# Optimization experiments

Hardware: AMD Instinct MI355X
Metric: run time of the kernel (lower is better)

## Reference

```python
import jax, jax.numpy as jnp
import numpy as np

WS = 2          # spatial window (patch) size
C = 96          # patch channels
IMG = 256       # image size
NS = IMG // WS  # 128 patches per side
N = NS * NS     # 16384 tokens
TD = C * WS * WS  # 384 token dim
H = 6           # heads
D = TD // H     # 64 head dim
W1 = 128        # one-sided attention window (attention_window=256 // 2)
G = 50          # num global tokens
NEG = -1e9
GPOS = np.linspace(0, N - 1, G).astype(np.int32)  # torch.linspace(...).long()


def setup_inputs() -> dict:
    key = jax.random.key(0)
    ks = jax.random.split(key, 13)
    s = 1.0 / np.sqrt(TD)
    def W(k):
        return jax.random.normal(k, (TD, TD), jnp.float32) * s
    def b(k):
        return jax.random.normal(k, (TD,), jnp.float32) * 0.02
    return {
        'x': jax.random.normal(ks[0], (2, C, IMG, IMG), jnp.float32),
        'Wq': W(ks[1]), 'bq': b(ks[2]),
        'Wk': W(ks[3]), 'bk': b(ks[4]),
        'Wv': W(ks[5]), 'bv': b(ks[6]),
        'Wqg': W(ks[7]), 'bqg': b(ks[8]),
        'Wkg': W(ks[9]), 'bkg': b(ks[10]),
        'Wvg': W(ks[11]), 'bvg': b(ks[12]),
    }


def _tokens(x):
    # (B,C,IMG,IMG) -> (B,N,TD); matches unfold/permute/view of the torch code
    B = x.shape[0]
    t = x.reshape(B, C, NS, WS, NS, WS).transpose(0, 1, 2, 4, 3, 5)  # B,C,ns,ns,ws,ws
    t = t.reshape(B, C, N, WS * WS).transpose(0, 2, 1, 3)
    return t.reshape(B, N, TD)


def _untokens(o):
    B = o.shape[0]
    o = o.reshape(B, NS, NS, C, WS, WS).transpose(0, 3, 1, 4, 2, 5)
    return o.reshape(B, C, IMG, IMG)


def _heads(t):
    B = t.shape[0]
    return t.reshape(B, -1, H, D).transpose(0, 2, 1, 3)  # (B,H,S,D)


def _longformer(tokens, Wq, bq, Wk, bk, Wv, bv, Wqg, bqg, Wkg, bkg, Wvg, bvg):
    B = tokens.shape[0]
    scale = np.float32(1.0 / np.sqrt(D))
    q = _heads(tokens @ Wq + bq) * scale  # (B,H,N,D)
    k = _heads(tokens @ Wk + bk)
    v = _heads(tokens @ Wv + bv)

    nc = N // W1  # 128 chunks of size w
    qc = q.reshape(B, H, nc, W1, D)
    # overlapping key/value chunks of size 3w (prev | cur | next)
    kp = jnp.pad(k, ((0, 0), (0, 0), (W1, W1), (0, 0))).reshape(B, H, nc + 2, W1, D)
    vp = jnp.pad(v, ((0, 0), (0, 0), (W1, W1), (0, 0))).reshape(B, H, nc + 2, W1, D)
    k3 = jnp.concatenate([kp[:, :, :-2], kp[:, :, 1:-1], kp[:, :, 2:]], axis=3)  # (B,H,nc,3w,D)
    v3 = jnp.concatenate([vp[:, :, :-2], vp[:, :, 1:-1], vp[:, :, 2:]], axis=3)

    band = jnp.einsum('bhcqd,bhckd->bhcqk', qc, k3)  # (B,H,nc,w,3w)
    # banded validity: key within +-w of query, and inside [0,N)
    i = np.arange(W1)[:, None]
    j = np.arange(3 * W1)[None, :]
    rel = j - W1 - i
    relmask = (rel >= -W1) & (rel <= W1)  # (w,3w)
    absidx = np.arange(nc)[:, None] * W1 + np.arange(3 * W1)[None, :] - W1
    absmask = (absidx >= 0) & (absidx < N)  # (nc,3w)
    mask = jnp.asarray(relmask[None, :, :] & absmask[:, None, :])  # (nc,w,3w)
    band = jnp.where(mask[None, None], band, NEG)

    # global key columns seen by every (local) query
    kg = k[:, :, GPOS]  # (B,H,G,D)
    vg = v[:, :, GPOS]
    gsc = jnp.einsum('bhcqd,bhgd->bhcqg', qc, kg)  # (B,H,nc,w,G)

    probs = jax.nn.softmax(jnp.concatenate([gsc, band], axis=-1), axis=-1)
    out = jnp.einsum('bhcqg,bhgd->bhcqd', probs[..., :G], vg) \
        + jnp.einsum('bhcqk,bhckd->bhcqd', probs[..., G:], v3)
    out = out.reshape(B, H, N, D).transpose(0, 2, 1, 3).reshape(B, N, TD)

    # global-query full attention (separate projections), overwrite global rows
    qg = _heads((tokens[:, GPOS] @ Wqg + bqg)) * scale  # (B,H,G,D)
    kga = _heads(tokens @ Wkg + bkg)  # (B,H,N,D)
    vga = _heads(tokens @ Wvg + bvg)
    gp = jax.nn.softmax(jnp.einsum('bhgd,bhnd->bhgn', qg, kga), axis=-1)
    og = jnp.einsum('bhgn,bhnd->bhgd', gp, vga).transpose(0, 2, 1, 3).reshape(B, G, TD)
    return out.at[:, GPOS].set(og)


def reference(x, Wq, bq, Wk, bk, Wv, bv, Wqg, bqg, Wkg, bkg, Wvg, bvg):
    tokens = _tokens(x)
    out = _longformer(tokens, Wq, bq, Wk, bk, Wv, bv, Wqg, bqg, Wkg, bkg, Wvg, bvg)
    return _untokens(out)
```

## Files before the change

kernel.cpp:

```cpp
#include <hip/hip_runtime.h>

#define DEVI __device__ __forceinline__

typedef __bf16 v8bf __attribute__((ext_vector_type(8)));
typedef float f32x4 __attribute__((ext_vector_type(4)));
typedef int int4v __attribute__((ext_vector_type(4)));
typedef int int2v __attribute__((ext_vector_type(2)));

constexpr int B_  = 2;
constexpr int C_  = 96;
constexpr int IMG = 256;
constexpr int N_  = 16384;
constexpr int TD  = 384;
constexpr int H_  = 6;
constexpr int G_  = 50;

DEVI short f2bf(float f){
  unsigned u = __builtin_bit_cast(unsigned, f);
  u = (u + 0x7fffu + ((u >> 16) & 1u)) >> 16;
  return (short)u;
}
DEVI unsigned cvtpk(float lo, float hi){
  unsigned r;
  asm("v_cvt_pk_bf16_f32 %0, %1, %2" : "=v"(r) : "v"(lo), "v"(hi));
  return r;
}
DEVI int gpos(int g){ return (16383 * g) / 49; }

DEVI f32x4 mfma16(v8bf a, v8bf b, f32x4 c){
  return __builtin_amdgcn_mfma_f32_16x16x32_bf16(a, b, c, 0, 0, 0);
}

DEVI void gload16(const void* g, void* l){
  __builtin_amdgcn_global_load_lds((const __attribute__((address_space(1))) void*)g,
                                   (__attribute__((address_space(3))) void*)l, 16, 0, 0);
}

__global__ __launch_bounds__(256) void prep_w(
    const float* __restrict__ w0, const float* __restrict__ w1,
    const float* __restrict__ w2, const float* __restrict__ w3,
    const float* __restrict__ w4, const float* __restrict__ w5,
    short* __restrict__ Wt){
  __shared__ float sT[64][65];
  int z = blockIdx.y;
  const float* W = z==0 ? w0 : z==1 ? w1 : z==2 ? w2 : z==3 ? w3 : z==4 ? w4 : w5;
  int tile = blockIdx.x;
  int k0 = (tile / 6) * 64, n0 = (tile % 6) * 64;
  int t = threadIdx.x;
  int r = t >> 2, c0 = (t & 3) * 16;
  #pragma unroll
  for (int e = 0; e < 16; e += 4){
    f32x4 v = *reinterpret_cast<const f32x4*>(&W[(size_t)(k0+r)*TD + n0 + c0 + e]);
    #pragma unroll
    for (int i = 0; i < 4; i++) sT[r][c0 + e + i] = v[i];
  }
  __syncthreads();
  int rn = t >> 2, ck0 = (t & 3) * 16;
  short pk[16];
  #pragma unroll
  for (int e = 0; e < 16; e++) pk[e] = f2bf(sT[ck0 + e][rn]);
  short* dst = Wt + (size_t)z*TD*TD + (size_t)(n0+rn)*TD + k0 + ck0;
  *reinterpret_cast<int4v*>(dst)     = *reinterpret_cast<int4v*>(&pk[0]);
  *reinterpret_cast<int4v*>(dst + 8) = *reinterpret_cast<int4v*>(&pk[8]);
}

__global__ void tokenize(const float* __restrict__ x, short* __restrict__ tokens){
  int idx = blockIdx.x * 256 + threadIdx.x;
  int t8 = idx % (TD/8);
  int bn = idx / (TD/8);
  int n = bn % N_, b = bn / N_;
  int t0 = t8 * 8;
  int i0 = (n >> 7) * 2, j0 = (n & 127) * 2;
  short o[8];
  #pragma unroll
  for (int e = 0; e < 8; e++){
    int t = t0 + e;
    int c = t >> 2, wi = (t >> 1) & 1, wj = t & 1;
    o[e] = f2bf(x[((b*C_ + c)*IMG + i0 + wi)*IMG + j0 + wj]);
  }
  *reinterpret_cast<int4v*>(tokens + bn*TD + t0) = *reinterpret_cast<int4v*>(o);
}

__global__ void gather_tokg(const short* __restrict__ tokens, short* __restrict__ tokg){
  int idx = blockIdx.x*256 + threadIdx.x;
  int r = idx / 48, cb = (idx % 48)*8;
  int b = r >> 6, q = r & 63;
  int4v val = {};
  if (q < G_) val = *reinterpret_cast<const int4v*>(tokens + ((size_t)b*N_ + gpos(q))*TD + cb);
  *reinterpret_cast<int4v*>(tokg + r*TD + cb) = val;
}

__global__ __launch_bounds__(256) void gemm_proj(
    const short* __restrict__ A, const short* __restrict__ Wt,
    const float* __restrict__ bq, const float* __restrict__ bk, const float* __restrict__ bv,
    const float* __restrict__ bkg, const float* __restrict__ bvg,
    short* __restrict__ qbuf, short* __restrict__ kbuf, short* __restrict__ vT,
    short* __restrict__ kgabuf, short* __restrict__ vgaT)
{
  __shared__ short smem[16384];
  int lin = blockIdx.x;
  int id = (lin & 7)*480 + (lin >> 3);
  int mt = id / 15, r15 = id % 15;
  int by = r15 % 3, bz = r15 / 3;
  const float* bias = bz==0 ? bq : bz==1 ? bk : bz==2 ? bv : bz==3 ? bkg : bvg;
  const short* Wz = Wt + bz*TD*TD;
  int m0 = mt * 128, n0 = by * 128;
  int tid = threadIdx.x, l = tid & 63, w = tid >> 6;
  int wm = w >> 1, wn = w & 1;
  int q16 = l & 15, g4 = l >> 4;

  int st_r  = (l >> 2);
  int st_cg = ((l & 3) ^ ((l >> 3) & 3));
  auto STAGE = [&](int kt, int s){
    #pragma unroll
    for (int it = 0; it < 4; it++){
      int ch = w*4 + it;
      int c8 = ch & 7;
      int r_ = c8*16 + st_r;
      const short* src = (ch < 8)
        ? A  + (size_t)(m0+r_)*TD + kt*32 + st_cg*8
        : Wz + (size_t)(n0+r_)*TD + kt*32 + st_cg*8;
      gload16(src, smem + ((ch < 8) ? 0 : 8192) + s*4096 + c8*512);
    }
  };

  int fr = q16;
  int fcg = g4 ^ ((l >> 1) & 3);
  f32x4 acc[4][4] = {};
  bool trans = (bz == 2 || bz == 4);

  STAGE(0, 0);
  if (trans){
    #pragma unroll 2
    for (int t = 0; t < 12; t++){
      int cur = t & 1;
      if (t < 11){ STAGE(t+1, cur ^ 1); asm volatile("s_waitcnt vmcnt(4)" ::: "memory"); }
      else       { asm volatile("s_waitcnt vmcnt(0)" ::: "memory"); }
      __builtin_amdgcn_s_barrier();
      v8bf af[4], bfr[4];
      #pragma unroll
      for (int i = 0; i < 4; i++){
        af[i]  = *reinterpret_cast<const v8bf*>(&smem[       cur*4096 + (wm*64 + i*16 + fr)*32 + fcg*8]);
        bfr[i] = *reinterpret_cast<const v8bf*>(&smem[8192 + cur*4096 + (wn*64 + i*16 + fr)*32 + fcg*8]);
      }
      #pragma unroll
      for (int mi = 0; mi < 4; mi++)
        #pragma unroll
        for (int ni = 0; ni < 4; ni++)
          acc[mi][ni] = mfma16(af[mi], bfr[ni], acc[mi][ni]);
      asm volatile("s_waitcnt lgkmcnt(0)" ::: "memory");
      __builtin_amdgcn_s_barrier();
    }
    short* outT = (bz == 2) ? vT : vgaT;
    #pragma unroll
    for (int mi = 0; mi < 4; mi++){
      int n_base = wm*64 + mi*16 + g4*4;
      #pragma unroll
      for (int ni = 0; ni < 4; ni++){
        int t_local = wn*64 + ni*16 + q16;
        float bc = bias[n0 + t_local];
        short pk[4];
        #pragma unroll
        for (int jj = 0; jj < 4; jj++) pk[jj] = f2bf(acc[mi][ni][jj] + bc);
        int phys = t_local*128 + (((n_base >> 3) ^ (t_local & 15)) << 3) + (n_base & 7);
        *reinterpret_cast<int2v*>(&smem[phys]) = *reinterpret_cast<int2v*>(pk);
      }
    }
    __syncthreads();
    int b = mt >> 7;
    int nb = m0 & 16383;
    #pragma unroll
    for (int p = 0; p < 8; p++){
      int t = p*16 + (tid >> 4);
      int c8 = tid & 15;
      int4v val = *reinterpret_cast<const int4v*>(&smem[t*128 + ((c8 ^ (t & 15)) << 3)]);
      int h = (n0 + t) >> 6, d = (n0 + t) & 63;
      *reinterpret_cast<int4v*>(outT + ((size_t)((b*H_ + h)*64 + d))*N_ + nb + c8*8) = val;
    }
  } else {
    #pragma unroll 2
    for (int t = 0; t < 12; t++){
      int cur = t & 1;
      if (t < 11){ STAGE(t+1, cur ^ 1); asm volatile("s_waitcnt vmcnt(4)" ::: "memory"); }
      else       { asm volatile("s_waitcnt vmcnt(0)" ::: "memory"); }
      __builtin_amdgcn_s_barrier();
      v8bf af[4], bfr[4];
      #pragma unroll
      for (int i = 0; i < 4; i++){
        af[i]  = *reinterpret_cast<const v8bf*>(&smem[       cur*4096 + (wm*64 + i*16 + fr)*32 + fcg*8]);
        bfr[i] = *reinterpret_cast<const v8bf*>(&smem[8192 + cur*4096 + (wn*64 + i*16 + fr)*32 + fcg*8]);
      }
      #pragma unroll
      for (int mi = 0; mi < 4; mi++)
        #pragma unroll
        for (int ni = 0; ni < 4; ni++)
          acc[mi][ni] = mfma16(bfr[ni], af[mi], acc[mi][ni]);
      asm volatile("s_waitcnt lgkmcnt(0)" ::: "memory");
      __builtin_amdgcn_s_barrier();
    }
    short* out = bz==0 ? qbuf : bz==1 ? kbuf : kgabuf;
    float scale = (bz == 0) ? 0.125f : 1.0f;
    #pragma unroll
    for (int mi = 0; mi < 4; mi++){
      int tl = wm*64 + mi*16 + q16;
      int x = (tl & 7) << 1;
      #pragma unroll
      for (int ni = 0; ni < 4; ni++){
        int tdl = wn*64 + ni*16 + g4*4;
        f32x4 bvv = *reinterpret_cast<const f32x4*>(&bias[n0 + tdl]);
        short pk[4];
        #pragma unroll
        for (int jj = 0; jj < 4; jj++) pk[jj] = f2bf((acc[mi][ni][jj] + bvv[jj]) * scale);
        int c4 = (tdl >> 2) ^ x;
        *reinterpret_cast<int2v*>(&smem[tl*128 + c4*4]) = *reinterpret_cast<int2v*>(pk);
      }
    }
    __syncthreads();
    #pragma unroll
    for (int p = 0; p < 8; p++){
      int r = p*16 + (tid >> 4);
      int c16 = tid & 15;
      int c4 = (2*c16) ^ ((r & 7) << 1);
      int4v val = *reinterpret_cast<const int4v*>(&smem[r*128 + c4*4]);
      *reinterpret_cast<int4v*>(out + (size_t)(m0 + r)*TD + n0 + c16*8) = val;
    }
  }
}

__global__ __launch_bounds__(256) void gemm_qg(
    const short* __restrict__ A, const short* __restrict__ Wt,
    const float* __restrict__ bias, short* __restrict__ out)
{
  __shared__ short sA[128][72];
  __shared__ short sB[128][72];
  const short* Wz = Wt + 5*TD*TD;
  int n0 = blockIdx.x * 128;
  int tid = threadIdx.x, l = tid & 63, w = tid >> 6;
  int wm = w >> 1, wn = w & 1;
  f32x4 acc[4][4] = {};
  for (int k0 = 0; k0 < TD; k0 += 64){
    #pragma unroll
    for (int i = 0; i < 4; i++){
      int ch = i*256 + tid; int row = ch >> 3, cb = (ch & 7) * 8;
      *reinterpret_cast<int4v*>(&sA[row][cb]) = *reinterpret_cast<const int4v*>(A  + row*TD + k0 + cb);
      *reinterpret_cast<int4v*>(&sB[row][cb]) = *reinterpret_cast<const int4v*>(Wz + (n0+row)*TD + k0 + cb);
    }
    __syncthreads();
    #pragma unroll
    for (int ks = 0; ks < 2; ks++){
      v8bf af[4], bfr[4];
      #pragma unroll
      for (int i = 0; i < 4; i++){
        af[i]  = *reinterpret_cast<const v8bf*>(&sA[wm*64 + i*16 + (l&15)][ks*32 + (l>>4)*8]);
        bfr[i] = *reinterpret_cast<const v8bf*>(&sB[wn*64 + i*16 + (l&15)][ks*32 + (l>>4)*8]);
      }
      #pragma unroll
      for (int mi = 0; mi < 4; mi++)
        #pragma unroll
        for (int ni = 0; ni < 4; ni++)
          acc[mi][ni] = mfma16(af[mi], bfr[ni], acc[mi][ni]);
    }
    __syncthreads();
  }
  #pragma unroll
  for (int mi = 0; mi < 4; mi++){
    int row = wm*64 + mi*16 + (l>>4)*4;
    #pragma unroll
    for (int ni = 0; ni < 4; ni++){
      int col = n0 + wn*64 + ni*16 + (l&15);
      float bc = bias[col];
      #pragma unroll
      for (int jj = 0; jj < 4; jj++)
        out[(row+jj)*TD + col] = f2bf((acc[mi][ni][jj] + bc) * 0.125f);
    }
  }
}

__global__ void gather_gkv(const short* __restrict__ kbuf, const short* __restrict__ vT,
                           short* __restrict__ kg, short* __restrict__ vgTg){
  int bh = blockIdx.x; int b = bh / H_, h = bh % H_;
  int t = threadIdx.x;
  #pragma unroll
  for (int it = 0; it < 2; it++){
    int u = it*256 + t; int g = u >> 3, cc = (u & 7)*8;
    int4v val = {};
    if (g < G_) val = *reinterpret_cast<const int4v*>(kbuf + ((size_t)b*N_ + gpos(g))*TD + h*64 + cc);
    *reinterpret_cast<int4v*>(kg + (size_t)bh*4096 + g*64 + cc) = val;
  }
  #pragma unroll
  for (int it = 0; it < 16; it++){
    int u = it*256 + t; int d = u >> 6, g = u & 63;
    short val = 0;
    if (g < G_) val = vT[((size_t)bh*64 + d)*N_ + gpos(g)];
    vgTg[(size_t)bh*4096 + d*64 + g] = val;
  }
}

__global__ __launch_bounds__(512, 4) void band_attn(
    const short* __restrict__ qb, const short* __restrict__ kbuf, const short* __restrict__ vT,
    const short* __restrict__ kg, const short* __restrict__ vgTg,
    float* __restrict__ out)
{
  __shared__ short sK[448][64];
  __shared__ short sP[8][16][72];
  int lin = blockIdx.y*128 + blockIdx.x;
  int id = (lin & 7)*192 + (lin >> 3);
  int c = id & 127;
  int bh = id >> 7; int b = bh / H_, h = bh % H_;
  int tid = threadIdx.x, l = tid & 63, w = tid >> 6;
  int g4 = l >> 4, q16 = l & 15;
  int cb0 = c*128 - 128;

  #pragma unroll
  for (int it = 0; it < 7; it++){
    int ch = w*7 + it;
    int r = ch*8 + (l>>3);
    int cc = ((l & 7) ^ (l >> 3)) * 8;
    const short* src;
    if (ch < 8){
      src = kg + (size_t)bh*4096 + r*64 + cc;
    } else {
      int ka = cb0 + r - 64;
      ka = ka < 0 ? 0 : (ka > N_-1 ? N_-1 : ka);
      src = kbuf + ((size_t)b*N_ + ka)*TD + h*64 + cc;
    }
    gload16(src, &sK[ch*8][0]);
  }

  int qrow0 = c*128 + w*16;
  v8bf aq[2];
  #pragma unroll
  for (int s = 0; s < 2; s++)
    aq[s] = *reinterpret_cast<const v8bf*>(qb + ((size_t)b*N_ + qrow0 + q16)*TD + h*64 + s*32 + g4*8);

  __syncthreads();

  f32x4 o[4] = {};
  float mrun = -1e30f, lrun = 0.f;

  int sbase = w >> 2;
  for (int sidx = 0; sidx < 6; sidx++){
    bool isg = (sidx == 0);
    int s0b = (sbase + sidx - 1) * 64;
    int kabs0 = cb0 + s0b;
    if (!isg && (kabs0 < 0 || kabs0 >= N_)) continue;
    int rbase = isg ? 0 : 64 + s0b;
    v8bf bv0[4];
    #pragma unroll
    for (int cf = 0; cf < 4; cf++){
      const short* vsrc = isg
        ? vgTg + (size_t)bh*4096 + (cf*16 + q16)*64 + g4*8
        : vT + ((size_t)bh*64 + cf*16 + q16)*N_ + kabs0 + g4*8;
      bv0[cf] = *reinterpret_cast<const v8bf*>(vsrc);
    }
    v8bf bkf[4][2];
    #pragma unroll
    for (int kc = 0; kc < 4; kc++)
      #pragma unroll
      for (int s = 0; s < 2; s++)
        bkf[kc][s] = *reinterpret_cast<const v8bf*>(
            &sK[rbase + kc*16 + q16][(((s << 2) | g4) ^ (q16 & 7)) * 8]);
    f32x4 sc[4] = {};
    __builtin_amdgcn_s_setprio(1);
    #pragma unroll
    for (int kc = 0; kc < 4; kc++){
      sc[kc] = mfma16(bkf[kc][0], aq[0], sc[kc]);
      sc[kc] = mfma16(bkf[kc][1], aq[1], sc[kc]);
    }
    __builtin_amdgcn_s_setprio(0);
    if (isg){
      #pragma unroll
      for (int jj = 0; jj < 4; jj++)
        if (48 + g4*4 + jj >= G_) sc[3][jj] = -1e30f;
    } else {
      bool allv = (s0b >= w*16 + 15) && (s0b <= w*16 + 193);
      if (!allv){
        int i_ = w*16 + q16;
        #pragma unroll
        for (int kc = 0; kc < 4; kc++)
          #pragma unroll
          for (int jj = 0; jj < 4; jj++){
            int rel = s0b + kc*16 + g4*4 + jj - 128 - i_;
            if (rel < -128 || rel > 128) sc[kc][jj] = -1e30f;
          }
      }
    }
    float mk = -1e30f;
    #pragma unroll
    for (int kc = 0; kc < 4; kc++)
      #pragma unroll
      for (int jj = 0; jj < 4; jj++) mk = fmaxf(mk, sc[kc][jj]);
    mk = fmaxf(mk, __shfl_xor(mk, 16, 64));
    mk = fmaxf(mk, __shfl_xor(mk, 32, 64));
    float mnew = fmaxf(mrun, mk);
    float f_ = __expf(mrun - mnew);
    mrun = mnew;
    float s_ = 0.f;
    #pragma unroll
    for (int kc = 0; kc < 4; kc++){
      #pragma unroll
      for (int jj = 0; jj < 4; jj++){
        sc[kc][jj] = __expf(sc[kc][jj] - mnew);
        s_ += sc[kc][jj];
      }
      int2v pw = { (int)cvtpk(sc[kc][0], sc[kc][1]), (int)cvtpk(sc[kc][2], sc[kc][3]) };
      *reinterpret_cast<int2v*>(&sP[w][q16][kc*16 + g4*4]) = pw;
    }
    s_ += __shfl_xor(s_, 16, 64);
    s_ += __shfl_xor(s_, 32, 64);
    lrun = lrun*f_ + s_;
    #pragma unroll
    for (int cf = 0; cf < 4; cf++)
      #pragma unroll
      for (int jj = 0; jj < 4; jj++) o[cf][jj] *= f_;
    v8bf ap[2];
    #pragma unroll
    for (int s2 = 0; s2 < 2; s2++)
      ap[s2] = *reinterpret_cast<const v8bf*>(&sP[w][q16][s2*32 + g4*8]);
    v8bf bv1[4];
    #pragma unroll
    for (int cf = 0; cf < 4; cf++){
      const short* vsrc = isg
        ? vgTg + (size_t)bh*4096 + (cf*16 + q16)*64 + 32 + g4*8
        : vT + ((size_t)bh*64 + cf*16 + q16)*N_ + kabs0 + 32 + g4*8;
      bv1[cf] = *reinterpret_cast<const v8bf*>(vsrc);
    }
    __builtin_amdgcn_s_setprio(1);
    #pragma unroll
    for (int cf = 0; cf < 4; cf++) o[cf] = mfma16(bv0[cf], ap[0], o[cf]);
    #pragma unroll
    for (int cf = 0; cf < 4; cf++) o[cf] = mfma16(bv1[cf], ap[1], o[cf]);
    __builtin_amdgcn_s_setprio(0);
  }
  float inv = 1.0f / lrun;
  int n = qrow0 + q16;
  int i0 = (n >> 7)*2, j0 = (n & 127)*2;
  #pragma unroll
  for (int cf = 0; cf < 4; cf++)
    #pragma unroll
    for (int jj = 0; jj < 4; jj++){
      float val = o[cf][jj] * inv;
      int t_ = h*64 + cf*16 + g4*4 + jj;
      int cc = t_ >> 2, wi = (t_ >> 1) & 1, wj = t_ & 1;
      out[((b*C_ + cc)*IMG + i0 + wi)*IMG + j0 + wj] = val;
    }
}

__global__ __launch_bounds__(256) void gattn_partial(
    const short* __restrict__ qgb, const short* __restrict__ kga, const short* __restrict__ vgaT,
    float* __restrict__ gpart)
{
  __shared__ short sP[4][64][72];
  int bh = blockIdx.x; int b = bh / H_, h = bh % H_;
  int kc = blockIdx.y;
  int tid = threadIdx.x, l = tid & 63, w = tid >> 6;
  int g4 = l >> 4, q16 = l & 15;
  v8bf aq[4][2];
  #pragma unroll
  for (int rf = 0; rf < 4; rf++)
    #pragma unroll
    for (int s = 0; s < 2; s++)
      aq[rf][s] = *reinterpret_cast<const v8bf*>(qgb + (b*64 + rf*16 + q16)*TD + h*64 + s*32 + g4*8);
  f32x4 o[4][4] = {};
  float mrun[4], lrun[4];
  #pragma unroll
  for (int rf = 0; rf < 4; rf++){ mrun[rf] = -1e30f; lrun[rf] = 0.f; }
  int keybase = kc*512 + w*128;
  for (int st = 0; st < 2; st++){
    int key0 = keybase + st*64;
    v8bf bkf[4][2];
    #pragma unroll
    for (int kcf = 0; kcf < 4; kcf++)
      #pragma unroll
      for (int s = 0; s < 2; s++)
        bkf[kcf][s] = *reinterpret_cast<const v8bf*>(kga + ((size_t)b*N_ + key0 + kcf*16 + q16)*TD + h*64 + s*32 + g4*8);
    #pragma unroll
    for (int rf = 0; rf < 4; rf++){
      f32x4 sc[4] = {};
      #pragma unroll
      for (int kcf = 0; kcf < 4; kcf++){
        sc[kcf] = mfma16(bkf[kcf][0], aq[rf][0], sc[kcf]);
        sc[kcf] = mfma16(bkf[kcf][1], aq[rf][1], sc[kcf]);
      }
      float mk = -1e30f;
      #pragma unroll
      for (int kcf = 0; kcf < 4; kcf++)
        #pragma unroll
        for (int jj = 0; jj < 4; jj++) mk = fmaxf(mk, sc[kcf][jj]);
      mk = fmaxf(mk, __shfl_xor(mk, 16, 64));
      mk = fmaxf(mk, __shfl_xor(mk, 32, 64));
      float mnew = fmaxf(mrun[rf], mk);
      float f_ = __expf(mrun[rf] - mnew);
      mrun[rf] = mnew;
      float s_ = 0.f;
      #pragma unroll
      for (int kcf = 0; kcf < 4; kcf++){
        #pragma unroll
        for (int jj = 0; jj < 4; jj++){
          sc[kcf][jj] = __expf(sc[kcf][jj] - mnew);
          s_ += sc[kcf][jj];
        }
        int2v pw = { (int)cvtpk(sc[kcf][0], sc[kcf][1]), (int)cvtpk(sc[kcf][2], sc[kcf][3]) };
        *reinterpret_cast<int2v*>(&sP[w][rf*16 + q16][kcf*16 + g4*4]) = pw;
      }
      s_ += __shfl_xor(s_, 16, 64);
      s_ += __shfl_xor(s_, 32, 64);
      lrun[rf] = lrun[rf]*f_ + s_;
      #pragma unroll
      for (int cf = 0; cf < 4; cf++)
        #pragma unroll
        for (int jj = 0; jj < 4; jj++) o[rf][cf][jj] *= f_;
    }
    v8bf bv[4][2];
    #pragma unroll
    for (int cf = 0; cf < 4; cf++)
      #pragma unroll
      for (int s2 = 0; s2 < 2; s2++)
        bv[cf][s2] = *reinterpret_cast<const v8bf*>(vgaT + ((size_t)bh*64 + cf*16 + q16)*N_ + key0 + s2*32 + g4*8);
    #pragma unroll
    for (int rf = 0; rf < 4; rf++){
      v8bf ap[2];
      #pragma unroll
      for (int s2 = 0; s2 < 2; s2++)
        ap[s2] = *reinterpret_cast<const v8bf*>(&sP[w][rf*16 + q16][s2*32 + g4*8]);
      #pragma unroll
      for (int cf = 0; cf < 4; cf++){
        o[rf][cf] = mfma16(bv[cf][0], ap[0], o[rf][cf]);
        o[rf][cf] = mfma16(bv[cf][1], ap[1], o[rf][cf]);
      }
    }
  }
  float* base = gpart + (size_t)(bh*128 + kc*4 + w) * 4224;
  #pragma unroll
  for (int rf = 0; rf < 4; rf++){
    if (g4 == 0){ base[rf*16 + q16] = mrun[rf]; base[64 + rf*16 + q16] = lrun[rf]; }
    #pragma unroll
    for (int cf = 0; cf < 4; cf++)
      #pragma unroll
      for (int jj = 0; jj < 4; jj++)
        base[128 + (cf*16 + g4*4 + jj)*64 + rf*16 + q16] = o[rf][cf][jj];
  }
}

__global__ void gattn_combine(const float* __restrict__ gpart, float* __restrict__ out){
  int bh = blockIdx.x; int b = bh / H_, h = bh % H_;
  int t = threadIdx.x;
  int q = t & 63;
  int d = blockIdx.y*4 + (t >> 6);
  if (q >= G_) return;
  const float* pb = gpart + (size_t)bh * 128 * 4224;
  float M = -1e30f;
  for (int p = 0; p < 128; p++) M = fmaxf(M, pb[p*4224 + q]);
  float L = 0.f; float acc = 0.f;
  for (int p = 0; p < 128; p++){
    const float* pp = pb + p*4224;
    float wgt = __expf(pp[q] - M);
    L += pp[64 + q] * wgt;
    acc += pp[128 + d*64 + q] * wgt;
  }
  float invL = 1.0f / L;
  int n = gpos(q);
  int i0 = (n >> 7)*2, j0 = (n & 127)*2;
  int t_ = h*64 + d;
  int cc = t_ >> 2, wi = (t_ >> 1) & 1, wj = t_ & 1;
  out[((b*C_ + cc)*IMG + i0 + wi)*IMG + j0 + wj] = acc * invL;
}

extern "C" void kernel_launch(void* const* d_in, const int* in_sizes, int n_in,
                              void* d_out, int out_size, void* d_ws, size_t ws_size,
                              hipStream_t stream)
{
  (void)in_sizes; (void)n_in; (void)out_size; (void)ws_size;
  const float* x   = (const float*)d_in[0];
  const float* Wq  = (const float*)d_in[1];  const float* bq  = (const float*)d_in[2];
  const float* Wk  = (const float*)d_in[3];  const float* bk  = (const float*)d_in[4];
  const float* Wv  = (const float*)d_in[5];  const float* bv  = (const float*)d_in[6];
  const float* Wqg = (const float*)d_in[7];  const float* bqg = (const float*)d_in[8];
  const float* Wkg = (const float*)d_in[9];  const float* bkg = (const float*)d_in[10];
  const float* Wvg = (const float*)d_in[11]; const float* bvg = (const float*)d_in[12];
  float* out = (float*)d_out;

  short* ws = (short*)d_ws;
  const size_t SZ = (size_t)B_ * N_ * TD;
  short* tokens  = ws;
  short* Wt      = tokens  + SZ;
  short* tokg    = Wt      + (size_t)6*TD*TD;
  short* qgb     = tokg    + (size_t)128*TD;
  short* qbuf    = qgb     + (size_t)128*TD;
  short* kbuf    = qbuf    + SZ;
  short* kgabuf  = kbuf    + SZ;
  short* vT      = kgabuf  + SZ;
  short* vgaT    = vT      + SZ;
  short* kg      = vgaT    + SZ;
  short* vgTg    = kg      + (size_t)12*64*64;
  float* gpart   = (float*)tokens;

  prep_w<<<dim3(36,6), dim3(256), 0, stream>>>(Wq, Wk, Wv, Wkg, Wvg, Wqg, Wt);
  tokenize<<<dim3(6144), dim3(256), 0, stream>>>(x, tokens);
  gemm_proj<<<dim3(3840), dim3(256), 0, stream>>>(tokens, Wt, bq, bk, bv, bkg, bvg,
                                                  qbuf, kbuf, vT, kgabuf, vgaT);
  gather_tokg<<<dim3(24), dim3(256), 0, stream>>>(tokens, tokg);
  gemm_qg<<<dim3(3), dim3(256), 0, stream>>>(tokg, Wt, bqg, qgb);
  gather_gkv<<<dim3(12), dim3(256), 0, stream>>>(kbuf, vT, kg, vgTg);
  band_attn<<<dim3(128,12), dim3(512), 0, stream>>>(qbuf, kbuf, vT, kg, vgTg, out);
  gattn_partial<<<dim3(12,32), dim3(256), 0, stream>>>(qgb, kgabuf, vgaT, gpart);
  gattn_combine<<<dim3(12,16), dim3(256), 0, stream>>>(gpart, out);
}
```

Baseline: 239.8 us.

## Process two key blocks per softmax step with lazy rescale; halve global-attn partial splits

The band attention loop now handles two 64-key blocks per online-softmax step. That halves the max/sum reductions and the rescales of the output accumulator. Rescaling is skipped unless some lane's max grows by more than 8, which accepts slightly larger exponent values in exchange for fewer multiplies. The global-query partial kernel processes 1024 keys per block instead of 512 with half the grid, so the combine kernel reduces over 64 partials instead of 128. The risks are extra register pressure from the doubled score buffer and reduced parallelism in the partial kernel.

```diff
diff --git a/kernel.cpp b/kernel.cpp
--- a/kernel.cpp
+++ b/kernel.cpp
@@ -337,22 +337,10 @@
 
   f32x4 o[4] = {};
   float mrun = -1e30f, lrun = 0.f;
-
   int sbase = w >> 2;
-  for (int sidx = 0; sidx < 6; sidx++){
-    bool isg = (sidx == 0);
-    int s0b = (sbase + sidx - 1) * 64;
-    int kabs0 = cb0 + s0b;
-    if (!isg && (kabs0 < 0 || kabs0 >= N_)) continue;
-    int rbase = isg ? 0 : 64 + s0b;
-    v8bf bv0[4];
-    #pragma unroll
-    for (int cf = 0; cf < 4; cf++){
-      const short* vsrc = isg
-        ? vgTg + (size_t)bh*4096 + (cf*16 + q16)*64 + g4*8
-        : vT + ((size_t)bh*64 + cf*16 + q16)*N_ + kabs0 + g4*8;
-      bv0[cf] = *reinterpret_cast<const v8bf*>(vsrc);
-    }
+  int i_ = w*16 + q16;
+
+  auto QK = [&](int rbase, f32x4* sc){
     v8bf bkf[4][2];
     #pragma unroll
     for (int kc = 0; kc < 4; kc++)
@@ -360,7 +348,6 @@
       for (int s = 0; s < 2; s++)
         bkf[kc][s] = *reinterpret_cast<const v8bf*>(
             &sK[rbase + kc*16 + q16][(((s << 2) | g4) ^ (q16 & 7)) * 8]);
-    f32x4 sc[4] = {};
     __builtin_amdgcn_s_setprio(1);
     #pragma unroll
     for (int kc = 0; kc < 4; kc++){
@@ -368,69 +355,133 @@
       sc[kc] = mfma16(bkf[kc][1], aq[1], sc[kc]);
     }
     __builtin_amdgcn_s_setprio(0);
-    if (isg){
-      #pragma unroll
-      for (int jj = 0; jj < 4; jj++)
-        if (48 + g4*4 + jj >= G_) sc[3][jj] = -1e30f;
-    } else {
-      bool allv = (s0b >= w*16 + 15) && (s0b <= w*16 + 193);
+  };
+
+  for (int ph = 0; ph < 3; ph++){
+    int s0bA = (sbase + 2*ph - 1) * 64;
+    int s0bB = (sbase + 2*ph) * 64;
+    bool isgA = (ph == 0);
+    int kabsA = cb0 + s0bA, kabsB = cb0 + s0bB;
+    bool validA = isgA || (kabsA >= 0 && kabsA < N_);
+    bool validB = (kabsB >= 0 && kabsB < N_);
+    if (!validA && !validB) continue;
+
+    f32x4 sc[8];
+    const f32x4 negv = {-1e30f, -1e30f, -1e30f, -1e30f};
+    #pragma unroll
+    for (int j = 0; j < 8; j++) sc[j] = negv;
+
+    if (validA){
+      sc[0] = sc[1] = sc[2] = sc[3] = f32x4{0.f, 0.f, 0.f, 0.f};
+      QK(isgA ? 0 : 64 + s0bA, &sc[0]);
+      if (isgA){
+        #pragma unroll
+        for (int jj = 0; jj < 4; jj++)
+          if (48 + g4*4 + jj >= G_) sc[3][jj] = -1e30f;
+      } else {
+        bool allv = (s0bA >= w*16 + 15) && (s0bA <= w*16 + 193);
+        if (!allv){
+          #pragma unroll
+          for (int kc = 0; kc < 4; kc++)
+            #pragma unroll
+            for (int jj = 0; jj < 4; jj++){
+              int rel = s0bA + kc*16 + g4*4 + jj - 128 - i_;
+              if (rel < -128 || rel > 128) sc[kc][jj] = -1e30f;
+            }
+        }
+      }
+    }
+    if (validB){
+      sc[4] = sc[5] = sc[6] = sc[7] = f32x4{0.f, 0.f, 0.f, 0.f};
+      QK(64 + s0bB, &sc[4]);
+      bool allv = (s0bB >= w*16 + 15) && (s0bB <= w*16 + 193);
       if (!allv){
-        int i_ = w*16 + q16;
         #pragma unroll
         for (int kc = 0; kc < 4; kc++)
           #pragma unroll
           for (int jj = 0; jj < 4; jj++){
-            int rel = s0b + kc*16 + g4*4 + jj - 128 - i_;
-            if (rel < -128 || rel > 128) sc[kc][jj] = -1e30f;
+            int rel = s0bB + kc*16 + g4*4 + jj - 128 - i_;
+            if (rel < -128 || rel > 128) sc[4+kc][jj] = -1e30f;
           }
       }
     }
     float mk = -1e30f;
     #pragma unroll
-    for (int kc = 0; kc < 4; kc++)
-      #pragma unroll
-      for (int jj = 0; jj < 4; jj++) mk = fmaxf(mk, sc[kc][jj]);
+    for (int j = 0; j < 8; j++)
+      #pragma unroll
+      for (int jj = 0; jj < 4; jj++) mk = fmaxf(mk, sc[j][jj]);
     mk = fmaxf(mk, __shfl_xor(mk, 16, 64));
     mk = fmaxf(mk, __shfl_xor(mk, 32, 64));
-    float mnew = fmaxf(mrun, mk);
-    float f_ = __expf(mrun - mnew);
-    mrun = mnew;
+    if (__any(mk > mrun + 8.f)){
+      float mnew = fmaxf(mrun, mk);
+      float f_ = __expf(mrun - mnew);
+      mrun = mnew;
+      lrun *= f_;
+      #pragma unroll
+      for (int cf = 0; cf < 4; cf++)
+        #pragma unroll
+        for (int jj = 0; jj < 4; jj++) o[cf][jj] *= f_;
+    }
     float s_ = 0.f;
     #pragma unroll
-    for (int kc = 0; kc < 4; kc++){
+    for (int j = 0; j < 8; j++)
       #pragma unroll
       for (int jj = 0; jj < 4; jj++){
-        sc[kc][jj] = __expf(sc[kc][jj] - mnew);
-        s_ += sc[kc][jj];
-      }
-      int2v pw = { (int)cvtpk(sc[kc][0], sc[kc][1]), (int)cvtpk(sc[kc][2], sc[kc][3]) };
-      *reinterpret_cast<int2v*>(&sP[w][q16][kc*16 + g4*4]) = pw;
-    }
+        sc[j][jj] = __expf(sc[j][jj] - mrun);
+        s_ += sc[j][jj];
+      }
     s_ += __shfl_xor(s_, 16, 64);
     s_ += __shfl_xor(s_, 32, 64);
-    lrun = lrun*f_ + s_;
-    #pragma unroll
-    for (int cf = 0; cf < 4; cf++)
-      #pragma unroll
-      for (int jj = 0; jj < 4; jj++) o[cf][jj] *= f_;
-    v8bf ap[2];
-    #pragma unroll
-    for (int s2 = 0; s2 < 2; s2++)
-      ap[s2] = *reinterpret_cast<const v8bf*>(&sP[w][q16][s2*32 + g4*8]);
-    v8bf bv1[4];
-    #pragma unroll
-    for (int cf = 0; cf < 4; cf++){
-      const short* vsrc = isg
-        ? vgTg + (size_t)bh*4096 + (cf*16 + q16)*64 + 32 + g4*8
-        : vT + ((size_t)bh*64 + cf*16 + q16)*N_ + kabs0 + 32 + g4*8;
-      bv1[cf] = *reinterpret_cast<const v8bf*>(vsrc);
-    }
-    __builtin_amdgcn_s_setprio(1);
-    #pragma unroll
-    for (int cf = 0; cf < 4; cf++) o[cf] = mfma16(bv0[cf], ap[0], o[cf]);
-    #pragma unroll
-    for (int cf = 0; cf < 4; cf++) o[cf] = mfma16(bv1[cf], ap[1], o[cf]);
-    __builtin_amdgcn_s_setprio(0);
+    lrun += s_;
+    if (validA){
+      #pragma unroll
+      for (int kc = 0; kc < 4; kc++){
+        int2v pw = { (int)cvtpk(sc[kc][0], sc[kc][1]), (int)cvtpk(sc[kc][2], sc[kc][3]) };
+        *reinterpret_cast<int2v*>(&sP[w][q16][kc*16 + g4*4]) = pw;
+      }
+      v8bf ap[2];
+      #pragma unroll
+      for (int s2 = 0; s2 < 2; s2++)
+        ap[s2] = *reinterpret_cast<const v8bf*>(&sP[w][q16][s2*32 + g4*8]);
+      #pragma unroll
+      for (int s2 = 0; s2 < 2; s2++){
+        v8bf bv[4];
+        #pragma unroll
+        for (int cf = 0; cf < 4; cf++){
+          const short* vsrc = isgA
+            ? vgTg + (size_t)bh*4096 + (cf*16 + q16)*64 + s2*32 + g4*8
+            : vT + ((size_t)bh*64 + cf*16 + q16)*N_ + kabsA + s2*32 + g4*8;
+          bv[cf] = *reinterpret_cast<const v8bf*>(vsrc);
+        }
+        __builtin_amdgcn_s_setprio(1);
+        #pragma unroll
+        for (int cf = 0; cf < 4; cf++) o[cf] = mfma16(bv[cf], ap[s2], o[cf]);
+        __builtin_amdgcn_s_setprio(0);
+      }
+    }
+    if (validB){
+      #pragma unroll
+      for (int kc = 0; kc < 4; kc++){
+        int2v pw = { (int)cvtpk(sc[4+kc][0], sc[4+kc][1]), (int)cvtpk(sc[4+kc][2], sc[4+kc][3]) };
+        *reinterpret_cast<int2v*>(&sP[w][q16][kc*16 + g4*4]) = pw;
+      }
+      v8bf ap[2];
+      #pragma unroll
+      for (int s2 = 0; s2 < 2; s2++)
+        ap[s2] = *reinterpret_cast<const v8bf*>(&sP[w][q16][s2*32 + g4*8]);
+      #pragma unroll
+      for (int s2 = 0; s2 < 2; s2++){
+        v8bf bv[4];
+        #pragma unroll
+        for (int cf = 0; cf < 4; cf++)
+          bv[cf] = *reinterpret_cast<const v8bf*>(
+              vT + ((size_t)bh*64 + cf*16 + q16)*N_ + kabsB + s2*32 + g4*8);
+        __builtin_amdgcn_s_setprio(1);
+        #pragma unroll
+        for (int cf = 0; cf < 4; cf++) o[cf] = mfma16(bv[cf], ap[s2], o[cf]);
+        __builtin_amdgcn_s_setprio(0);
+      }
+    }
   }
   float inv = 1.0f / lrun;
   int n = qrow0 + q16;
@@ -465,8 +516,8 @@
   float mrun[4], lrun[4];
   #pragma unroll
   for (int rf = 0; rf < 4; rf++){ mrun[rf] = -1e30f; lrun[rf] = 0.f; }
-  int keybase = kc*512 + w*128;
-  for (int st = 0; st < 2; st++){
+  int keybase = kc*1024 + w*256;
+  for (int st = 0; st < 4; st++){
     int key0 = keybase + st*64;
     v8bf bkf[4][2];
     #pragma unroll
@@ -530,7 +581,7 @@
       }
     }
   }
-  float* base = gpart + (size_t)(bh*128 + kc*4 + w) * 4224;
+  float* base = gpart + (size_t)(bh*64 + kc*4 + w) * 4224;
   #pragma unroll
   for (int rf = 0; rf < 4; rf++){
     if (g4 == 0){ base[rf*16 + q16] = mrun[rf]; base[64 + rf*16 + q16] = lrun[rf]; }
@@ -548,11 +599,11 @@
   int q = t & 63;
   int d = blockIdx.y*4 + (t >> 6);
   if (q >= G_) return;
-  const float* pb = gpart + (size_t)bh * 128 * 4224;
+  const float* pb = gpart + (size_t)bh * 64 * 4224;
   float M = -1e30f;
-  for (int p = 0; p < 128; p++) M = fmaxf(M, pb[p*4224 + q]);
+  for (int p = 0; p < 64; p++) M = fmaxf(M, pb[p*4224 + q]);
   float L = 0.f; float acc = 0.f;
-  for (int p = 0; p < 128; p++){
+  for (int p = 0; p < 64; p++){
     const float* pp = pb + p*4224;
     float wgt = __expf(pp[q] - M);
     L += pp[64 + q] * wgt;
@@ -603,6 +654,6 @@
   gemm_qg<<<dim3(3), dim3(256), 0, stream>>>(tokg, Wt, bqg, qgb);
   gather_gkv<<<dim3(12), dim3(256), 0, stream>>>(kbuf, vT, kg, vgTg);
   band_attn<<<dim3(128,12), dim3(512), 0, stream>>>(qbuf, kbuf, vT, kg, vgTg, out);
-  gattn_partial<<<dim3(12,32), dim3(256), 0, stream>>>(qgb, kgabuf, vgaT, gpart);
+  gattn_partial<<<dim3(12,16), dim3(256), 0, stream>>>(qgb, kgabuf, vgaT, gpart);
   gattn_combine<<<dim3(12,16), dim3(256), 0, stream>>>(gpart, out);
 }
```

Result: faster. 229.5 us (-4.3%).
